# Kernel tuning notes

Measured on AMD Instinct MI355X. Metric: run time of the kernel, lower is better.

The kernel has to match this reference:

```python
import jax, jax.numpy as jnp
import numpy as np

# Dims: S strings, B batch, D bond dim, N=784 input sites, P=2 phys dim, L=10 labels
S, B, D, N, P, L = 4, 64, 32, 784, 2, 10
HALF = N // 2  # 392 sites on each side of the label node


def setup_inputs() -> dict:
    key = jax.random.key(0)
    ks = jax.random.split(key, 6)
    # scale chosen so each transfer-matrix step keeps vector norm ~O(1)
    std = (3.0 / (2.0 * D)) ** 0.5
    inputs = jax.random.uniform(ks[0], (B, N, P), dtype=jnp.float32)
    A_first = jax.random.normal(ks[1], (S, D, P), dtype=jnp.float32) * std          # node 0
    A_left = jax.random.normal(ks[2], (S, HALF - 1, D, P, D), dtype=jnp.float32) * std   # nodes 1..391
    A_label = jax.random.normal(ks[3], (S, D, L, D), dtype=jnp.float32) * std       # node 392 (open label edge)
    A_right = jax.random.normal(ks[4], (S, HALF - 1, D, P, D), dtype=jnp.float32) * std  # nodes 393..783
    A_last = jax.random.normal(ks[5], (S, D, P), dtype=jnp.float32) * std           # node 784
    return {"inputs": inputs, "A_first": A_first, "A_left": A_left,
            "A_label": A_label, "A_right": A_right, "A_last": A_last}


def reference(inputs, A_first, A_left, A_label, A_right, A_last):
    x = inputs  # (B, N, P); original reshapes each sample to (784, 2)
    # Contract physical legs with inputs -> per-site transfer matrices, site-major for scan
    Ml = jnp.einsum('snipj,bnp->nsbij', A_left, x[:, 1:HALF])      # (391, S, B, D, D)
    v0 = jnp.einsum('sdp,bp->sbd', A_first, x[:, 0])               # (S, B, D)

    def step_left(v, M):
        return jnp.einsum('sbi,sbij->sbj', v, M), None
    v, _ = jax.lax.scan(step_left, v0, Ml)                          # (S, B, D)

    T = jnp.einsum('sbd,sdlj->sblj', v, A_label)                    # (S, B, L, D)

    Mr = jnp.einsum('snipj,bnp->nsbij', A_right, x[:, HALF:N - 1])  # (391, S, B, D, D)
    r0 = jnp.einsum('sdp,bp->sbd', A_last, x[:, N - 1])             # (S, B, D)

    def step_right(r, M):
        return jnp.einsum('sbij,sbj->sbi', M, r), None
    r, _ = jax.lax.scan(step_right, r0, Mr, reverse=True)           # (S, B, D)

    out_per_string = jnp.einsum('sblj,sbj->sbl', T, r)              # (S, B, L)
    # forward multiplies the per-string 10-vectors elementwise (init ones)
    return jnp.prod(out_per_string, axis=0)                         # (B, L)
```

## Files before the change

kernel.cpp:

```cpp
#include <hip/hip_runtime.h>
#include <stdint.h>

#define S 4
#define B 64
#define D 32
#define N 784
#define P 2
#define L 10
#define HALF 392
#define NSTEP 391
#define NPAIR 196
#define SLICE 4096

typedef float f4 __attribute__((ext_vector_type(4)));
typedef float f2 __attribute__((ext_vector_type(2)));

__device__ __forceinline__ float bcast(float v, int lane) {
    return __uint_as_float(__builtin_amdgcn_readlane(__float_as_uint(v), lane));
}

__global__ __launch_bounds__(256) void pair_kernel(
    const float* __restrict__ A_left, const float* __restrict__ A_right,
    const float* __restrict__ x,
    float* __restrict__ Wbuf, float* __restrict__ wtab)
{
    const int stream = blockIdx.x;
    const int t      = blockIdx.y;
    const int side   = stream >> 2, s = stream & 3;
    __shared__ float sA[2048], sB[2048];
    const int tid = threadIdx.x;
    const bool leftover = (t == 195);

    const float* As = (side ? A_right : A_left) + (size_t)s * (NSTEP * 2048);
    int ia, ib;
    if (side == 0) { ia = 2 * t; ib = 2 * t + 1; }
    else           { ia = 389 - 2 * t; ib = 390 - 2 * t; }
    if (leftover)  { ia = side ? 0 : 390; ib = ia; }

    const float4* ga = (const float4*)(As + (size_t)ia * 2048);
    const float4* gb = (const float4*)(As + (size_t)ib * 2048);
    ((float4*)sA)[tid] = ga[tid]; ((float4*)sA)[tid + 256] = ga[tid + 256];
    ((float4*)sB)[tid] = gb[tid]; ((float4*)sB)[tid + 256] = gb[tid + 256];
    __syncthreads();

    const int c = tid >> 6, rest = tid & 63, ff = rest >> 1, eh = rest & 1;
    const int a = c & 1, bb = c >> 1;
    float out[16];

    if (!leftover) {
        if (side == 0) {
            float col[32];
            #pragma unroll
            for (int k = 0; k < 32; ++k) col[k] = sB[k * 64 + bb * 32 + ff];
            #pragma unroll
            for (int e0 = 0; e0 < 16; ++e0) {
                const int e = eh * 16 + e0; float acc = 0.f;
                #pragma unroll
                for (int k = 0; k < 32; ++k)
                    acc = fmaf(sA[e * 64 + a * 32 + k], col[k], acc);
                out[e0] = acc;
            }
        } else {
            float row[32];
            #pragma unroll
            for (int k = 0; k < 32; ++k) row[k] = sA[ff * 64 + a * 32 + k];
            #pragma unroll
            for (int e0 = 0; e0 < 16; ++e0) {
                const int e = eh * 16 + e0; float acc = 0.f;
                #pragma unroll
                for (int k = 0; k < 32; ++k)
                    acc = fmaf(row[k], sB[k * 64 + bb * 32 + e], acc);
                out[e0] = acc;
            }
        }
    } else {
        #pragma unroll
        for (int e0 = 0; e0 < 16; ++e0) {
            const int e = eh * 16 + e0;
            out[e0] = (side == 0) ? sA[e * 64 + a * 32 + ff]
                                  : sA[ff * 64 + a * 32 + e];
        }
    }

    float* Wt = Wbuf + ((size_t)stream * NPAIR + t) * SLICE;
    #pragma unroll
    for (int q0 = 0; q0 < 4; ++q0) {
        const int qq = eh * 4 + q0;
        float4 val = make_float4(out[q0 * 4 + 0], out[q0 * 4 + 1],
                                 out[q0 * 4 + 2], out[q0 * 4 + 3]);
        ((float4*)Wt)[(bb * 8 + qq) * 64 + a * 32 + ff] = val;
    }

    if (stream < 2 && tid < 64) {
        const int sd = stream;
        const float2* x2 = (const float2*)x;
        float2 xa, xb;
        if (!leftover) {
            int na, nb;
            if (sd == 0) { na = 2 * t + 1; nb = 2 * t + 2; }
            else         { int ma = 389 - 2 * t; na = HALF + ma; nb = na + 1; }
            xa = x2[(size_t)tid * N + na];
            xb = x2[(size_t)tid * N + nb];
        } else {
            xa = x2[(size_t)tid * N + (sd ? HALF : 391)];
            xb = make_float2(1.f, 0.f);
        }
        float4 w = make_float4(xa.x * xb.x, xa.y * xb.x, xa.x * xb.y, xa.y * xb.y);
        ((float4*)wtab)[((size_t)sd * 64 + tid) * NPAIR + t] = w;
    }
}

#define GLOADX4(dst, voff, base, off) \
    asm volatile("global_load_dwordx4 %0, %1, %2 offset:" #off \
                 : "=v"(dst) : "v"(voff), "s"(base))

#define ISSUE_SLOT(SL) do { \
    GLOADX4(SL##0,  voff, base0, 0); GLOADX4(SL##1,  voff, base0, 1024); \
    GLOADX4(SL##2,  voff, base0, 2048); GLOADX4(SL##3,  voff, base0, 3072); \
    GLOADX4(SL##4,  voff, base1, 0); GLOADX4(SL##5,  voff, base1, 1024); \
    GLOADX4(SL##6,  voff, base1, 2048); GLOADX4(SL##7,  voff, base1, 3072); \
    GLOADX4(SL##8,  voff, base2, 0); GLOADX4(SL##9,  voff, base2, 1024); \
    GLOADX4(SL##10, voff, base2, 2048); GLOADX4(SL##11, voff, base2, 3072); \
    GLOADX4(SL##12, voff, base3, 0); GLOADX4(SL##13, voff, base3, 1024); \
    GLOADX4(SL##14, voff, base3, 2048); GLOADX4(SL##15, voff, base3, 3072); \
    voff += 16384; \
} while (0)

#define WAIT(n) do { \
    asm volatile("s_waitcnt vmcnt(" #n ")"); \
    __builtin_amdgcn_sched_barrier(0); \
} while (0)

#define FMAQUAD(SLl, SLh, QAL, QAH, QBL, QBH, EB) do { \
    const f2 l0 = __builtin_shufflevector(SLl, SLl, 0, 1); \
    const f2 l1 = __builtin_shufflevector(SLl, SLl, 2, 3); \
    const f2 h0 = __builtin_shufflevector(SLh, SLh, 0, 1); \
    const f2 h1 = __builtin_shufflevector(SLh, SLh, 2, 3); \
    f2 sa0, sb0, sa1, sb1; \
    sa0.x = bcast(v0, EB + 0); sa0.y = bcast(v0, EB + 1); \
    sb0.x = bcast(v1, EB + 0); sb0.y = bcast(v1, EB + 1); \
    QAL = __builtin_elementwise_fma(l0, sa0, QAL); \
    QAH = __builtin_elementwise_fma(h0, sa0, QAH); \
    QBL = __builtin_elementwise_fma(l0, sb0, QBL); \
    QBH = __builtin_elementwise_fma(h0, sb0, QBH); \
    sa1.x = bcast(v0, EB + 2); sa1.y = bcast(v0, EB + 3); \
    sb1.x = bcast(v1, EB + 2); sb1.y = bcast(v1, EB + 3); \
    QAL = __builtin_elementwise_fma(l1, sa1, QAL); \
    QAH = __builtin_elementwise_fma(h1, sa1, QAH); \
    QBL = __builtin_elementwise_fma(l1, sb1, QBL); \
    QBH = __builtin_elementwise_fma(h1, sb1, QBH); \
} while (0)

#define CONSUME_SLOT(SL, W0, W1) do { \
    f2 Q00 = {0.f, 0.f}, Q01 = {0.f, 0.f}, Q02 = {0.f, 0.f}, Q03 = {0.f, 0.f}; \
    f2 Q10 = {0.f, 0.f}, Q11 = {0.f, 0.f}, Q12 = {0.f, 0.f}, Q13 = {0.f, 0.f}; \
    FMAQUAD(SL##0, SL##8,  Q00, Q02, Q10, Q12, 0); \
    FMAQUAD(SL##1, SL##9,  Q00, Q02, Q10, Q12, 4); \
    FMAQUAD(SL##2, SL##10, Q00, Q02, Q10, Q12, 8); \
    FMAQUAD(SL##3, SL##11, Q00, Q02, Q10, Q12, 12); \
    FMAQUAD(SL##4, SL##12, Q01, Q03, Q11, Q13, 16); \
    FMAQUAD(SL##5, SL##13, Q01, Q03, Q11, Q13, 20); \
    FMAQUAD(SL##6, SL##14, Q01, Q03, Q11, Q13, 24); \
    FMAQUAD(SL##7, SL##15, Q01, Q03, Q11, Q13, 28); \
    const float q00 = Q00.x + Q00.y, q01 = Q01.x + Q01.y; \
    const float q02 = Q02.x + Q02.y, q03 = Q03.x + Q03.y; \
    const float q10 = Q10.x + Q10.y, q11 = Q11.x + Q11.y; \
    const float q12 = Q12.x + Q12.y, q13 = Q13.x + Q13.y; \
    const float wl0 = c2 ? W0.y : W0.x, wh0 = c2 ? W0.w : W0.z; \
    const float wl1 = c2 ? W1.y : W1.x, wh1 = c2 ? W1.w : W1.z; \
    const float part0 = fmaf(wl0, q00 + q01, wh0 * (q02 + q03)); \
    const float part1 = fmaf(wl1, q10 + q11, wh1 * (q12 + q13)); \
    v0 = part0 + __shfl_xor(part0, 32); \
    v1 = part1 + __shfl_xor(part1, 32); \
} while (0)

__global__ __attribute__((amdgpu_waves_per_eu(1, 1))) __launch_bounds__(64, 1)
void chain_kernel(
    const float* __restrict__ x,
    const float* __restrict__ A_first, const float* __restrict__ A_last,
    const float* __restrict__ Wbuf, const float* __restrict__ wtab,
    float* __restrict__ ws_v)
{
    __shared__ float4 lw[2 * NPAIR];

    const int lane = threadIdx.x, c2 = lane >> 5, f = lane & 31;
    const int blk = blockIdx.x, stream = blk & 7;
    const int side = stream >> 2, s = stream & 3;
    const int bp = blk >> 3;
    const int b0 = 2 * bp, b1 = 2 * bp + 1;

    const float4* wt4 = (const float4*)wtab;
    for (int i = lane; i < NPAIR; i += 64) {
        lw[2 * i]     = wt4[((size_t)side * 64 + b0) * NPAIR + i];
        lw[2 * i + 1] = wt4[((size_t)side * 64 + b1) * NPAIR + i];
    }

    const float2* x2 = (const float2*)x;
    const int site0 = side ? (N - 1) : 0;
    const float2 af  = ((const float2*)(side ? A_last : A_first))[s * D + f];
    const float2 xx0 = x2[(size_t)b0 * N + site0];
    const float2 xx1 = x2[(size_t)b1 * N + site0];
    float v0 = fmaf(af.x, xx0.x, af.y * xx0.y);
    float v1 = fmaf(af.x, xx1.x, af.y * xx1.y);

    const uint64_t wbase = (uint64_t)((const char*)Wbuf
                         + (size_t)stream * (NPAIR * SLICE) * 4);
    const uint64_t base0 = wbase, base1 = wbase + 4096;
    const uint64_t base2 = wbase + 8192, base3 = wbase + 12288;
    uint32_t voff = (uint32_t)lane * 16;

    f4 A0,A1,A2,A3,A4,A5,A6,A7,A8,A9,A10,A11,A12,A13,A14,A15;
    f4 B0,B1,B2,B3,B4,B5,B6,B7,B8,B9,B10,B11,B12,B13,B14,B15;

    ISSUE_SLOT(A);
    ISSUE_SLOT(B);
    float4 wA0 = lw[0], wA1 = lw[1];
    float4 wB0 = lw[2], wB1 = lw[3];

    for (int k = 0; k < 97; ++k) {
        WAIT(16); CONSUME_SLOT(A, wA0, wA1);
        ISSUE_SLOT(A);
        wA0 = lw[2 * (2 * k + 2)]; wA1 = lw[2 * (2 * k + 2) + 1];
        WAIT(16); CONSUME_SLOT(B, wB0, wB1);
        ISSUE_SLOT(B);
        wB0 = lw[2 * (2 * k + 3)]; wB1 = lw[2 * (2 * k + 3) + 1];
    }
    WAIT(16); CONSUME_SLOT(A, wA0, wA1);
    WAIT(0);  CONSUME_SLOT(B, wB0, wB1);

    if (lane < 32) {
        ws_v[(side * S + s) * (B * D) + b0 * D + f] = v0;
        ws_v[(side * S + s) * (B * D) + b1 * D + f] = v1;
    }
}

__global__ __launch_bounds__(64) void chain_fb(
    const float* __restrict__ x, const float* __restrict__ A_first,
    const float* __restrict__ A_left, const float* __restrict__ A_right,
    const float* __restrict__ A_last, float* __restrict__ ws_v)
{
    const int blk = blockIdx.x, pair = blk & 7, b = blk >> 3;
    const int side = pair >> 2, s = pair & 3;
    const int lane = threadIdx.x, p = lane >> 5, j = lane & 31;
    const float* xb = x + b * (N * P);
    float v;
    if (side == 0) {
        v = fmaf(A_first[s*D*P + j*P + 0], xb[0], A_first[s*D*P + j*P + 1] * xb[1]);
        const float* Abase = A_left + (size_t)s * (NSTEP * D * P * D);
        for (int n = 1; n <= NSTEP; ++n) {
            const float* M = Abase + (n - 1) * (D * P * D) + p * D + j;
            const float x0 = xb[n*P], x1 = xb[n*P + 1];
            float t0 = 0.f, t1 = 0.f;
            #pragma unroll
            for (int i = 0; i < D; i += 2) {
                t0 = fmaf(bcast(v, i),     M[i * (P*D)],       t0);
                t1 = fmaf(bcast(v, i + 1), M[(i + 1) * (P*D)], t1);
            }
            const float t = t0 + t1, o = __shfl_xor(t, 32);
            v = (p == 0) ? fmaf(x0, t, x1 * o) : fmaf(x1, t, x0 * o);
        }
    } else {
        v = fmaf(A_last[s*D*P + j*P + 0], xb[(N-1)*P], A_last[s*D*P + j*P + 1] * xb[(N-1)*P + 1]);
        const float* Abase = A_right + (size_t)s * (NSTEP * D * P * D);
        for (int m = NSTEP - 1; m >= 0; --m) {
            const float4* R4 = (const float4*)(Abase + m * (D*P*D) + j * (P*D) + p * D);
            const float x0 = xb[(HALF+m)*P], x1 = xb[(HALF+m)*P + 1];
            float t0 = 0.f, t1 = 0.f;
            #pragma unroll
            for (int q = 0; q < 8; ++q) {
                const float4 rv = R4[q];
                t0 = fmaf(rv.x, bcast(v, 4*q+0), t0);
                t1 = fmaf(rv.y, bcast(v, 4*q+1), t1);
                t0 = fmaf(rv.z, bcast(v, 4*q+2), t0);
                t1 = fmaf(rv.w, bcast(v, 4*q+3), t1);
            }
            const float t = t0 + t1, o = __shfl_xor(t, 32);
            v = (p == 0) ? fmaf(x0, t, x1 * o) : fmaf(x1, t, x0 * o);
        }
    }
    if (p == 0) ws_v[(side*S + s)*(B*D) + b*D + j] = v;
}

__global__ __launch_bounds__(64) void label_prod_kernel(
    const float* __restrict__ ws_v, const float* __restrict__ A_label,
    float* __restrict__ out)
{
    const int b = blockIdx.x;
    const int lane = threadIdx.x, h = lane >> 5, j = lane & 31;
    float pr0 = 1.f, pr1 = 1.f, pr2 = 1.f, pr3 = 1.f, pr4 = 1.f;

    #pragma unroll
    for (int s = 0; s < S; ++s) {
        const float vj = ws_v[(0 * S + s) * (B * D) + b * D + j];
        const float rj = ws_v[(1 * S + s) * (B * D) + b * D + j];
        #pragma unroll
        for (int q = 0; q < 5; ++q) {
            const int l = h * 5 + q;
            float w = 0.f;
            #pragma unroll
            for (int d = 0; d < D; ++d)
                w = fmaf(bcast(vj, d), A_label[((s * D + d) * L + l) * D + j], w);
            float c = w * rj;
            c += __shfl_xor(c, 1); c += __shfl_xor(c, 2); c += __shfl_xor(c, 4);
            c += __shfl_xor(c, 8); c += __shfl_xor(c, 16);
            if (q == 0) pr0 *= c; else if (q == 1) pr1 *= c;
            else if (q == 2) pr2 *= c; else if (q == 3) pr3 *= c; else pr4 *= c;
        }
    }
    if (j == 0) {
        out[b * L + h * 5 + 0] = pr0;
        out[b * L + h * 5 + 1] = pr1;
        out[b * L + h * 5 + 2] = pr2;
        out[b * L + h * 5 + 3] = pr3;
        out[b * L + h * 5 + 4] = pr4;
    }
}

extern "C" void kernel_launch(void* const* d_in, const int* in_sizes, int n_in,
                              void* d_out, int out_size, void* d_ws, size_t ws_size,
                              hipStream_t stream) {
    const float* x       = (const float*)d_in[0];
    const float* A_first = (const float*)d_in[1];
    const float* A_left  = (const float*)d_in[2];
    const float* A_label = (const float*)d_in[3];
    const float* A_right = (const float*)d_in[4];
    const float* A_last  = (const float*)d_in[5];
    float* out = (float*)d_out;

    float* ws_v = (float*)d_ws;
    float* wtab = ws_v + 2 * S * B * D;
    float* Wbuf = wtab + 2 * 64 * NPAIR * 4;
    const size_t need = (size_t)(16384 + 100352 + 8 * NPAIR * SLICE) * 4;

    if (ws_size >= need) {
        pair_kernel<<<dim3(8, NPAIR), dim3(256), 0, stream>>>(A_left, A_right, x, Wbuf, wtab);
        chain_kernel<<<dim3(256), dim3(64), 0, stream>>>(x, A_first, A_last, Wbuf, wtab, ws_v);
    } else {
        chain_fb<<<dim3(2 * S * B), dim3(64), 0, stream>>>(x, A_first, A_left, A_right, A_last, ws_v);
    }
    label_prod_kernel<<<dim3(B), dim3(64), 0, stream>>>(ws_v, A_label, out);
}
```

Before: 113.3 us.

## Process one batch item per chain block and launch twice as many blocks

The chain kernel now handles one batch sample per wavefront instead of two, so the grid grows from 256 to 512 single-wave blocks and each wave does half the FMAs and readlane broadcasts per step. The occupancy hint is raised to two waves per EU to let two chain waves share a SIMD. The cost is that each shared matrix slice is now streamed from memory by twice as many waves, doubling the load traffic per step, whereas before one load fed two samples. The serial latency chain per step gets shorter, which should help a latency-bound recurrence.

```diff
diff --git a/kernel.cpp b/kernel.cpp
--- a/kernel.cpp
+++ b/kernel.cpp
@@ -131,77 +131,60 @@
     __builtin_amdgcn_sched_barrier(0); \
 } while (0)
 
-#define FMAQUAD(SLl, SLh, QAL, QAH, QBL, QBH, EB) do { \
+#define FMAQUAD(SLl, SLh, QAL, QAH, EB) do { \
     const f2 l0 = __builtin_shufflevector(SLl, SLl, 0, 1); \
     const f2 l1 = __builtin_shufflevector(SLl, SLl, 2, 3); \
     const f2 h0 = __builtin_shufflevector(SLh, SLh, 0, 1); \
     const f2 h1 = __builtin_shufflevector(SLh, SLh, 2, 3); \
-    f2 sa0, sb0, sa1, sb1; \
+    f2 sa0, sa1; \
     sa0.x = bcast(v0, EB + 0); sa0.y = bcast(v0, EB + 1); \
-    sb0.x = bcast(v1, EB + 0); sb0.y = bcast(v1, EB + 1); \
     QAL = __builtin_elementwise_fma(l0, sa0, QAL); \
     QAH = __builtin_elementwise_fma(h0, sa0, QAH); \
-    QBL = __builtin_elementwise_fma(l0, sb0, QBL); \
-    QBH = __builtin_elementwise_fma(h0, sb0, QBH); \
     sa1.x = bcast(v0, EB + 2); sa1.y = bcast(v0, EB + 3); \
-    sb1.x = bcast(v1, EB + 2); sb1.y = bcast(v1, EB + 3); \
     QAL = __builtin_elementwise_fma(l1, sa1, QAL); \
     QAH = __builtin_elementwise_fma(h1, sa1, QAH); \
-    QBL = __builtin_elementwise_fma(l1, sb1, QBL); \
-    QBH = __builtin_elementwise_fma(h1, sb1, QBH); \
 } while (0)
 
-#define CONSUME_SLOT(SL, W0, W1) do { \
+#define CONSUME_SLOT(SL, W0) do { \
     f2 Q00 = {0.f, 0.f}, Q01 = {0.f, 0.f}, Q02 = {0.f, 0.f}, Q03 = {0.f, 0.f}; \
-    f2 Q10 = {0.f, 0.f}, Q11 = {0.f, 0.f}, Q12 = {0.f, 0.f}, Q13 = {0.f, 0.f}; \
-    FMAQUAD(SL##0, SL##8,  Q00, Q02, Q10, Q12, 0); \
-    FMAQUAD(SL##1, SL##9,  Q00, Q02, Q10, Q12, 4); \
-    FMAQUAD(SL##2, SL##10, Q00, Q02, Q10, Q12, 8); \
-    FMAQUAD(SL##3, SL##11, Q00, Q02, Q10, Q12, 12); \
-    FMAQUAD(SL##4, SL##12, Q01, Q03, Q11, Q13, 16); \
-    FMAQUAD(SL##5, SL##13, Q01, Q03, Q11, Q13, 20); \
-    FMAQUAD(SL##6, SL##14, Q01, Q03, Q11, Q13, 24); \
-    FMAQUAD(SL##7, SL##15, Q01, Q03, Q11, Q13, 28); \
+    FMAQUAD(SL##0, SL##8,  Q00, Q02, 0); \
+    FMAQUAD(SL##1, SL##9,  Q00, Q02, 4); \
+    FMAQUAD(SL##2, SL##10, Q00, Q02, 8); \
+    FMAQUAD(SL##3, SL##11, Q00, Q02, 12); \
+    FMAQUAD(SL##4, SL##12, Q01, Q03, 16); \
+    FMAQUAD(SL##5, SL##13, Q01, Q03, 20); \
+    FMAQUAD(SL##6, SL##14, Q01, Q03, 24); \
+    FMAQUAD(SL##7, SL##15, Q01, Q03, 28); \
     const float q00 = Q00.x + Q00.y, q01 = Q01.x + Q01.y; \
     const float q02 = Q02.x + Q02.y, q03 = Q03.x + Q03.y; \
-    const float q10 = Q10.x + Q10.y, q11 = Q11.x + Q11.y; \
-    const float q12 = Q12.x + Q12.y, q13 = Q13.x + Q13.y; \
     const float wl0 = c2 ? W0.y : W0.x, wh0 = c2 ? W0.w : W0.z; \
-    const float wl1 = c2 ? W1.y : W1.x, wh1 = c2 ? W1.w : W1.z; \
     const float part0 = fmaf(wl0, q00 + q01, wh0 * (q02 + q03)); \
-    const float part1 = fmaf(wl1, q10 + q11, wh1 * (q12 + q13)); \
     v0 = part0 + __shfl_xor(part0, 32); \
-    v1 = part1 + __shfl_xor(part1, 32); \
 } while (0)
 
-__global__ __attribute__((amdgpu_waves_per_eu(1, 1))) __launch_bounds__(64, 1)
+__global__ __attribute__((amdgpu_waves_per_eu(2, 2))) __launch_bounds__(64, 2)
 void chain_kernel(
     const float* __restrict__ x,
     const float* __restrict__ A_first, const float* __restrict__ A_last,
     const float* __restrict__ Wbuf, const float* __restrict__ wtab,
     float* __restrict__ ws_v)
 {
-    __shared__ float4 lw[2 * NPAIR];
+    __shared__ float4 lw[NPAIR];
 
     const int lane = threadIdx.x, c2 = lane >> 5, f = lane & 31;
     const int blk = blockIdx.x, stream = blk & 7;
     const int side = stream >> 2, s = stream & 3;
-    const int bp = blk >> 3;
-    const int b0 = 2 * bp, b1 = 2 * bp + 1;
+    const int b = blk >> 3;
 
     const float4* wt4 = (const float4*)wtab;
-    for (int i = lane; i < NPAIR; i += 64) {
-        lw[2 * i]     = wt4[((size_t)side * 64 + b0) * NPAIR + i];
-        lw[2 * i + 1] = wt4[((size_t)side * 64 + b1) * NPAIR + i];
-    }
+    for (int i = lane; i < NPAIR; i += 64)
+        lw[i] = wt4[((size_t)side * 64 + b) * NPAIR + i];
 
     const float2* x2 = (const float2*)x;
     const int site0 = side ? (N - 1) : 0;
     const float2 af  = ((const float2*)(side ? A_last : A_first))[s * D + f];
-    const float2 xx0 = x2[(size_t)b0 * N + site0];
-    const float2 xx1 = x2[(size_t)b1 * N + site0];
+    const float2 xx0 = x2[(size_t)b * N + site0];
     float v0 = fmaf(af.x, xx0.x, af.y * xx0.y);
-    float v1 = fmaf(af.x, xx1.x, af.y * xx1.y);
 
     const uint64_t wbase = (uint64_t)((const char*)Wbuf
                          + (size_t)stream * (NPAIR * SLICE) * 4);
@@ -209,29 +192,27 @@
     const uint64_t base2 = wbase + 8192, base3 = wbase + 12288;
     uint32_t voff = (uint32_t)lane * 16;
 
-    f4 A0,A1,A2,A3,A4,A5,A6,A7,A8,A9,A10,A11,A12,A13,A14,A15;
-    f4 B0,B1,B2,B3,B4,B5,B6,B7,B8,B9,B10,B11,B12,B13,B14,B15;
-
-    ISSUE_SLOT(A);
-    ISSUE_SLOT(B);
-    float4 wA0 = lw[0], wA1 = lw[1];
-    float4 wB0 = lw[2], wB1 = lw[3];
+    f4 KA0,KA1,KA2,KA3,KA4,KA5,KA6,KA7,KA8,KA9,KA10,KA11,KA12,KA13,KA14,KA15;
+    f4 KB0,KB1,KB2,KB3,KB4,KB5,KB6,KB7,KB8,KB9,KB10,KB11,KB12,KB13,KB14,KB15;
+
+    ISSUE_SLOT(KA);
+    ISSUE_SLOT(KB);
+    float4 wA0 = lw[0];
+    float4 wB0 = lw[1];
 
     for (int k = 0; k < 97; ++k) {
-        WAIT(16); CONSUME_SLOT(A, wA0, wA1);
-        ISSUE_SLOT(A);
-        wA0 = lw[2 * (2 * k + 2)]; wA1 = lw[2 * (2 * k + 2) + 1];
-        WAIT(16); CONSUME_SLOT(B, wB0, wB1);
-        ISSUE_SLOT(B);
-        wB0 = lw[2 * (2 * k + 3)]; wB1 = lw[2 * (2 * k + 3) + 1];
-    }
-    WAIT(16); CONSUME_SLOT(A, wA0, wA1);
-    WAIT(0);  CONSUME_SLOT(B, wB0, wB1);
-
-    if (lane < 32) {
-        ws_v[(side * S + s) * (B * D) + b0 * D + f] = v0;
-        ws_v[(side * S + s) * (B * D) + b1 * D + f] = v1;
-    }
+        WAIT(16); CONSUME_SLOT(KA, wA0);
+        ISSUE_SLOT(KA);
+        wA0 = lw[2 * k + 2];
+        WAIT(16); CONSUME_SLOT(KB, wB0);
+        ISSUE_SLOT(KB);
+        wB0 = lw[2 * k + 3];
+    }
+    WAIT(16); CONSUME_SLOT(KA, wA0);
+    WAIT(0);  CONSUME_SLOT(KB, wB0);
+
+    if (lane < 32)
+        ws_v[(side * S + s) * (B * D) + b * D + f] = v0;
 }
 
 __global__ __launch_bounds__(64) void chain_fb(
@@ -334,7 +315,7 @@
 
     if (ws_size >= need) {
         pair_kernel<<<dim3(8, NPAIR), dim3(256), 0, stream>>>(A_left, A_right, x, Wbuf, wtab);
-        chain_kernel<<<dim3(256), dim3(64), 0, stream>>>(x, A_first, A_last, Wbuf, wtab, ws_v);
+        chain_kernel<<<dim3(512), dim3(64), 0, stream>>>(x, A_first, A_last, Wbuf, wtab, ws_v);
     } else {
         chain_fb<<<dim3(2 * S * B), dim3(64), 0, stream>>>(x, A_first, A_left, A_right, A_last, ws_v);
     }
```

Result: faster. 99.29 us, median of 2 (-12.4%).
